# Kernel tuning notes

Hardware: AMD Instinct MI355X
Metric: run time of the kernel (lower is better)

The kernel has to match this reference:

```python
import jax, jax.numpy as jnp
import numpy as np

KEEP_PROB = 0.3
KH, KW = 3, 3
STRIDE = (1, 1)
PADDING = ((1, 1), (1, 1))
DILATION = (1, 1)


def setup_inputs() -> dict:
    key = jax.random.key(0)
    k_x, k_w, k_m, k_b = jax.random.split(key, 4)
    B, C_in, H, W = 16, 64, 112, 112
    C_out = 128
    K = C_in * KH * KW  # 576
    x = jax.random.normal(k_x, (B, C_in, H, W), dtype=jnp.float32)
    weight = jax.random.normal(k_w, (C_out, K), dtype=jnp.float32)
    # binary sparsity pattern of the COO tensor, as a float mask
    mask = (jax.random.uniform(k_m, (C_out, K)) < KEEP_PROB).astype(jnp.float32)
    bias = jax.random.normal(k_b, (C_out,), dtype=jnp.float32)
    return {"x": x, "weight": weight, "mask": mask, "bias": bias}


def reference(x, weight, mask, bias):
    # Effective sparse weight matrix [C_out, C_in*kH*kW]
    spW = weight * mask
    # im2col (F.unfold): patches -> [B, C_in*kH*kW, H_out, W_out]
    # ordering of the K axis is (c, i, j) channel-major, matching torch unfold
    patches = jax.lax.conv_general_dilated_patches(
        x,
        filter_shape=(KH, KW),
        window_strides=STRIDE,
        padding=PADDING,
        rhs_dilation=DILATION,
    )  # [B, K, H_out, W_out]
    # sparse.mm(spW, X) + fold(1x1)  ==  GEMM over the K axis
    out = jnp.einsum('ok,bkhw->bohw', spW, patches)
    out = out + bias[None, :, None, None]
    return out
```

## Files before the change

### kernel.cpp

```cpp
#include <hip/hip_runtime.h>
#include <hip/hip_bf16.h>

#define C_IN    64
#define C_OUT   128
#define HH      112
#define WW      112
#define NB      16
#define KTOT    576
#define NSTEPS  36
#define NPIX    (HH*WW)
#define PH      114
#define PPIX    (PH*PH)
#define XT_OFF  147456
#define XT_BYTES ((size_t)NB * PPIX * C_IN * 2)
#define BAND_H  14
#define BH_X    18
#define B_RECS  288
#define A_BYTES 73728
#define B_BYTES 36864
#define TY      8
#define TX      16
#define HALO_X  18
#define HALO_P  180
#define TILES_X 7
#define NTILES  98

typedef __bf16 bf16x8 __attribute__((ext_vector_type(8)));
typedef float  f32x16 __attribute__((ext_vector_type(16)));

static __device__ __forceinline__ unsigned short f2bf(float v) {
    unsigned int u = __builtin_bit_cast(unsigned int, v);
    u = u + 0x7fffu + ((u >> 16) & 1u);
    return (unsigned short)(u >> 16);
}

#define GLOAD_LDS(gp, lp) __builtin_amdgcn_global_load_lds( \
    (const __attribute__((address_space(1))) void*)(gp),    \
    (__attribute__((address_space(3))) void*)(lp), 16, 0, 0)

__global__ __launch_bounds__(256) void pack_w_kernel(
        const float* __restrict__ weight, const float* __restrict__ mask,
        unsigned short* __restrict__ pw) {
    int t  = blockIdx.x;
    int mt = threadIdx.x >> 6;
    int l  = threadIdx.x & 63;
    int g  = l >> 5;
    int m  = mt * 32 + (l & 31);
    unsigned int words[4];
    #pragma unroll
    for (int ew = 0; ew < 4; ++ew) {
        unsigned int w2[2];
        #pragma unroll
        for (int h = 0; h < 2; ++h) {
            int e    = ew * 2 + h;
            int klog = t * 16 + g * 8 + e;
            int ij   = klog >> 6;
            int c    = klog & 63;
            int ko   = c * 9 + ij;
            w2[h] = f2bf(weight[m * KTOT + ko] * mask[m * KTOT + ko]);
        }
        words[ew] = w2[0] | (w2[1] << 16);
    }
    uint4 o4; o4.x = words[0]; o4.y = words[1]; o4.z = words[2]; o4.w = words[3];
    ((uint4*)pw)[(t * 4 + mt) * 64 + l] = o4;
}

__global__ __launch_bounds__(256) void transpose_x_kernel(
        const float* __restrict__ x, unsigned short* __restrict__ xT) {
    const int b  = blockIdx.y;
    const int pp = blockIdx.x * 256 + threadIdx.x;
    if (pp >= PPIX) return;
    const int hp = pp / PH, wp = pp - hp * PH;
    const int gh = hp - 1, gw = wp - 1;
    const bool valid = (unsigned)gh < (unsigned)HH && (unsigned)gw < (unsigned)WW;
    const float* src = x + (size_t)b * C_IN * (HH * WW) + (gh * WW + gw);
    uint4* dst = (uint4*)(xT + ((size_t)b * PPIX + pp) * C_IN);
    #pragma unroll
    for (int cb = 0; cb < 8; ++cb) {
        unsigned int w4[4];
        #pragma unroll
        for (int h = 0; h < 4; ++h) {
            float v0 = valid ? src[(size_t)(cb * 8 + h * 2    ) * (HH * WW)] : 0.0f;
            float v1 = valid ? src[(size_t)(cb * 8 + h * 2 + 1) * (HH * WW)] : 0.0f;
            w4[h] = (unsigned)f2bf(v0) | ((unsigned)f2bf(v1) << 16);
        }
        uint4 o; o.x = w4[0]; o.y = w4[1]; o.z = w4[2]; o.w = w4[3];
        dst[cb] = o;
    }
}

__global__ __launch_bounds__(448, 1) void sparse_conv_band_kernel(
        const unsigned short* __restrict__ xT, const unsigned short* __restrict__ pw,
        const float* __restrict__ bias, float* __restrict__ out) {
    __shared__ __align__(16) unsigned char smem[A_BYTES + 2 * B_BYTES];
    unsigned char* As  = smem;
    unsigned char* Bs0 = smem + A_BYTES;
    unsigned char* Bs1 = smem + A_BYTES + B_BYTES;

    const int bid  = (blockIdx.x & 7) * 32 + (blockIdx.x >> 3);
    const int b    = bid >> 4;
    const int rem  = bid & 15;
    const int mh   = rem & 1;
    const int band = rem >> 1;
    const int h0   = band * BAND_H;
    const int tid  = threadIdx.x;
    const int wave = tid >> 6, l = tid & 63;
    const int g = l >> 5, ln = l & 31;

    const char* xTb = (const char*)xT + (size_t)b * PPIX * (C_IN * 2);

    {
        const char* pwb = (const char*)pw;
        #pragma unroll
        for (int r = 0; r < 10; ++r) {
            int c  = r * 448 + tid;
            int t  = c >> 7;
            int mt = (c >> 6) & 1;
            int ll = c & 63;
            const char* gp = pwb + (size_t)((t * 4 + mh * 2 + mt) * 64 + ll) * 16;
            GLOAD_LDS(gp, (char*)As + r * 7168 + wave * 1024);
        }
        if (tid < 128) {
            int c  = 10 * 448 + tid;
            int t  = c >> 7;
            int mt = (c >> 6) & 1;
            int ll = c & 63;
            const char* gp = pwb + (size_t)((t * 4 + mh * 2 + mt) * 64 + ll) * 16;
            GLOAD_LDS(gp, (char*)As + 10 * 7168 + wave * 1024);
        }
    }

    auto STAGE = [&](int it, unsigned char* dst) {
        const int w0 = it * 16;
        #pragma unroll
        for (int r = 0; r < 5; ++r) {
            int chunk = r * 448 + tid;
            int p = chunk >> 3, s = chunk & 7;
            int yy = p / BH_X, xx = p - yy * BH_X;
            const char* gp = xTb + (size_t)((h0 + yy) * PH + (w0 + xx)) * (C_IN * 2)
                                 + (((s ^ p) & 7) << 4);
            GLOAD_LDS(gp, (char*)dst + r * 7168 + wave * 1024);
        }
        if (tid < 64) {
            int chunk = 5 * 448 + tid;
            int p = chunk >> 3, s = chunk & 7;
            int yy = p / BH_X, xx = p - yy * BH_X;
            const char* gp = xTb + (size_t)((h0 + yy) * PH + (w0 + xx)) * (C_IN * 2)
                                 + (((s ^ p) & 7) << 4);
            GLOAD_LDS(gp, (char*)dst + 5 * 7168 + wave * 1024);
        }
    };

    const int py = 2 * wave + (ln >> 4);
    const int px = ln & 15;

    float bv[2][16];
    #pragma unroll
    for (int mt = 0; mt < 2; ++mt)
        #pragma unroll
        for (int r = 0; r < 16; ++r) {
            int mloc = (r & 3) + 8 * (r >> 2) + 4 * g;
            bv[mt][r] = bias[mh * 64 + mt * 32 + mloc];
        }

    STAGE(0, Bs0);
    __syncthreads();

    const size_t outb = (size_t)b * C_OUT * NPIX;

    #pragma unroll 1
    for (int it = 0; it < 7; ++it) {
        unsigned char* curB = (it & 1) ? Bs1 : Bs0;
        unsigned char* nxtB = (it & 1) ? Bs0 : Bs1;
        if (it < 6) STAGE(it + 1, nxtB);

        f32x16 acc[2];
        #pragma unroll
        for (int mt = 0; mt < 2; ++mt)
            #pragma unroll
            for (int r = 0; r < 16; ++r) acc[mt][r] = bv[mt][r];

        #pragma unroll
        for (int t = 0; t < NSTEPS; ++t) {
            const int ij = t >> 2, cs = t & 3;
            const int di = ij / 3, dj = ij - di * 3;
            const int jb = cs * 2 + g;
            bf16x8 a0 = __builtin_bit_cast(bf16x8,
                *(const uint4*)(As + ((t * 2 + 0) * 64 + l) * 16));
            bf16x8 a1 = __builtin_bit_cast(bf16x8,
                *(const uint4*)(As + ((t * 2 + 1) * 64 + l) * 16));
            const int Pa = (py + di) * BH_X + (px + dj);
            bf16x8 bb = __builtin_bit_cast(bf16x8,
                *(const uint4*)(curB + Pa * 128 + (((jb ^ Pa) & 7) << 4)));
            acc[0] = __builtin_amdgcn_mfma_f32_32x32x16_bf16(a0, bb, acc[0], 0, 0, 0);
            acc[1] = __builtin_amdgcn_mfma_f32_32x32x16_bf16(a1, bb, acc[1], 0, 0, 0);
        }

        #pragma unroll
        for (int mt = 0; mt < 2; ++mt)
            #pragma unroll
            for (int r = 0; r < 16; ++r) {
                int mloc = (r & 3) + 8 * (r >> 2) + 4 * g;
                int o = mh * 64 + mt * 32 + mloc;
                out[outb + (size_t)o * NPIX + (h0 + py) * WW + it * 16 + px] = acc[mt][r];
            }

        if (it < 6) __syncthreads();
    }
}

__global__ __launch_bounds__(256, 4) void sparse_conv_fb_kernel(
        const float* __restrict__ x, const unsigned short* __restrict__ pw,
        const float* __restrict__ bias, float* __restrict__ out) {
    __shared__ __align__(16) unsigned short xs[HALO_P * C_IN];

    const int bid = blockIdx.x;
    const int b   = bid / NTILES;
    const int t98 = bid % NTILES;
    const int tyi = t98 / TILES_X;
    const int txi = t98 % TILES_X;
    const int h0  = tyi * TY, w0 = txi * TX;
    const int tid = threadIdx.x;

    const float* xb = x + (size_t)b * C_IN * HH * WW;
    {
        const int p  = tid;
        const bool act = p < HALO_P;
        int yy = p / HALO_X;
        int xx = p - yy * HALO_X;
        int gh = h0 + yy - 1, gw = w0 + xx - 1;
        const bool valid = act && (unsigned)gh < (unsigned)HH && (unsigned)gw < (unsigned)WW;
        const float* bp = xb + (gh * WW + gw);
        float v[C_IN];
        #pragma unroll
        for (int c = 0; c < C_IN; ++c)
            v[c] = valid ? bp[c * (HH * WW)] : 0.0f;
        if (act) {
            char* xc = (char*)xs + p * (C_IN * 2);
            #pragma unroll
            for (int j = 0; j < 8; ++j) {
                bf16x8 bvv;
                #pragma unroll
                for (int e = 0; e < 8; ++e) bvv[e] = (__bf16)v[j * 8 + e];
                *(uint4*)(xc + (((j ^ p) & 7) << 4)) = __builtin_bit_cast(uint4, bvv);
            }
        }
    }
    __syncthreads();

    const int wave = tid >> 6, l = tid & 63;
    const int wm = wave >> 1, wn = wave & 1;
    const int g  = l >> 5,  ln = l & 31;

    int P0[2];
    #pragma unroll
    for (int ntp = 0; ntp < 2; ++ntp) {
        int pt = wn * 64 + ntp * 32 + ln;
        P0[ntp] = (pt >> 4) * HALO_X + (pt & 15);
    }

    f32x16 acc[2][2];
    #pragma unroll
    for (int i = 0; i < 2; ++i)
        #pragma unroll
        for (int jq = 0; jq < 2; ++jq)
            #pragma unroll
            for (int q = 0; q < 16; ++q) acc[i][jq][q] = 0.0f;

    const uint4* __restrict__ pwv = (const uint4*)pw;

    #pragma unroll 1
    for (int ij = 0; ij < 9; ++ij) {
        const int di = ij / 3;
        const int dj = ij - di * 3;
        const int P0a = P0[0] + di * HALO_X + dj;
        const int P1a = P0[1] + di * HALO_X + dj;
        #pragma unroll
        for (int cs = 0; cs < 4; ++cs) {
            const int t = ij * 4 + cs;
            bf16x8 a0 = __builtin_bit_cast(bf16x8, pwv[(t * 4 + wm * 2 + 0) * 64 + l]);
            bf16x8 a1 = __builtin_bit_cast(bf16x8, pwv[(t * 4 + wm * 2 + 1) * 64 + l]);
            const int jb = cs * 2 + g;
            bf16x8 b0 = __builtin_bit_cast(bf16x8,
                *(const uint4*)((const char*)xs + P0a * (C_IN * 2) + (((jb ^ P0a) & 7) << 4)));
            bf16x8 b1 = __builtin_bit_cast(bf16x8,
                *(const uint4*)((const char*)xs + P1a * (C_IN * 2) + (((jb ^ P1a) & 7) << 4)));
            acc[0][0] = __builtin_amdgcn_mfma_f32_32x32x16_bf16(a0, b0, acc[0][0], 0, 0, 0);
            acc[0][1] = __builtin_amdgcn_mfma_f32_32x32x16_bf16(a0, b1, acc[0][1], 0, 0, 0);
            acc[1][0] = __builtin_amdgcn_mfma_f32_32x32x16_bf16(a1, b0, acc[1][0], 0, 0, 0);
            acc[1][1] = __builtin_amdgcn_mfma_f32_32x32x16_bf16(a1, b1, acc[1][1], 0, 0, 0);
        }
    }

    const size_t outb = (size_t)b * C_OUT * HH * WW;
    #pragma unroll
    for (int mtp = 0; mtp < 2; ++mtp) {
        #pragma unroll
        for (int r = 0; r < 16; ++r) {
            int mloc = (r & 3) + 8 * (r >> 2) + 4 * g;
            int o = (wm * 2 + mtp) * 32 + mloc;
            float bvv = bias[o];
            #pragma unroll
            for (int ntp = 0; ntp < 2; ++ntp) {
                int p  = wn * 64 + ntp * 32 + ln;
                int gh = h0 + (p >> 4), gw = w0 + (p & 15);
                out[outb + ((size_t)o * HH + gh) * WW + gw] = acc[mtp][ntp][r] + bvv;
            }
        }
    }
}

extern "C" void kernel_launch(void* const* d_in, const int* in_sizes, int n_in,
                              void* d_out, int out_size, void* d_ws, size_t ws_size,
                              hipStream_t stream) {
    const float* x    = (const float*)d_in[0];
    const float* w    = (const float*)d_in[1];
    const float* mk   = (const float*)d_in[2];
    const float* bs   = (const float*)d_in[3];
    float* out        = (float*)d_out;
    unsigned short* pw = (unsigned short*)d_ws;

    pack_w_kernel<<<dim3(NSTEPS), dim3(256), 0, stream>>>(w, mk, pw);

    if (ws_size >= (size_t)XT_OFF + XT_BYTES) {
        unsigned short* xT = (unsigned short*)((char*)d_ws + XT_OFF);
        transpose_x_kernel<<<dim3((PPIX + 255) / 256, NB), dim3(256), 0, stream>>>(x, xT);
        sparse_conv_band_kernel<<<dim3(256), dim3(448), 0, stream>>>(xT, pw, bs, out);
    } else {
        sparse_conv_fb_kernel<<<dim3(NB * NTILES), dim3(256), 0, stream>>>(x, pw, bs, out);
    }
}
```

Baseline: 72.24 us.

## Split output channels into quarters, keep weights in registers, widen transpose parallelism

The main conv kernel now gives each block a quarter of the output channels (32) rather than half. Each lane holds its 36 weight fragments in VGPRs, so the 72KB LDS weight buffer is gone and only the double-buffered input band stays in LDS. The grid doubles to 512 blocks for better CU coverage, but every input band is now staged twice as often and each B fragment feeds one MFMA instead of two. The weight packing is changed to a row-major layout, and the transpose kernel uses 8 threads per padded pixel for more parallelism.

```diff
diff --git a/kernel.cpp b/kernel.cpp
--- a/kernel.cpp
+++ b/kernel.cpp
@@ -16,7 +16,6 @@
 #define BAND_H  14
 #define BH_X    18
 #define B_RECS  288
-#define A_BYTES 73728
 #define B_BYTES 36864
 #define TY      8
 #define TX      16
@@ -41,94 +40,68 @@
 __global__ __launch_bounds__(256) void pack_w_kernel(
         const float* __restrict__ weight, const float* __restrict__ mask,
         unsigned short* __restrict__ pw) {
-    int t  = blockIdx.x;
-    int mt = threadIdx.x >> 6;
-    int l  = threadIdx.x & 63;
-    int g  = l >> 5;
-    int m  = mt * 32 + (l & 31);
-    unsigned int words[4];
-    #pragma unroll
-    for (int ew = 0; ew < 4; ++ew) {
-        unsigned int w2[2];
-        #pragma unroll
-        for (int h = 0; h < 2; ++h) {
-            int e    = ew * 2 + h;
-            int klog = t * 16 + g * 8 + e;
-            int ij   = klog >> 6;
-            int c    = klog & 63;
-            int ko   = c * 9 + ij;
-            w2[h] = f2bf(weight[m * KTOT + ko] * mask[m * KTOT + ko]);
-        }
-        words[ew] = w2[0] | (w2[1] << 16);
-    }
-    uint4 o4; o4.x = words[0]; o4.y = words[1]; o4.z = words[2]; o4.w = words[3];
-    ((uint4*)pw)[(t * 4 + mt) * 64 + l] = o4;
+    const int m   = blockIdx.x;
+    const int tid = threadIdx.x;
+    #pragma unroll
+    for (int base = 0; base < 512; base += 256) {
+        int klog = base + tid;
+        int c = klog & 63, ij = klog >> 6;
+        int ko = c * 9 + ij;
+        pw[m * KTOT + klog] = f2bf(weight[m * KTOT + ko] * mask[m * KTOT + ko]);
+    }
+    if (tid < 64) {
+        int klog = 512 + tid;
+        int c = klog & 63, ij = klog >> 6;
+        int ko = c * 9 + ij;
+        pw[m * KTOT + klog] = f2bf(weight[m * KTOT + ko] * mask[m * KTOT + ko]);
+    }
 }
 
 __global__ __launch_bounds__(256) void transpose_x_kernel(
         const float* __restrict__ x, unsigned short* __restrict__ xT) {
-    const int b  = blockIdx.y;
-    const int pp = blockIdx.x * 256 + threadIdx.x;
-    if (pp >= PPIX) return;
-    const int hp = pp / PH, wp = pp - hp * PH;
+    const int b   = blockIdx.y;
+    const int idx = blockIdx.x * 256 + threadIdx.x;
+    if (idx >= PPIX * 8) return;
+    const int rec = idx >> 3, s = idx & 7;
+    const int hp = rec / PH, wp = rec - hp * PH;
     const int gh = hp - 1, gw = wp - 1;
     const bool valid = (unsigned)gh < (unsigned)HH && (unsigned)gw < (unsigned)WW;
-    const float* src = x + (size_t)b * C_IN * (HH * WW) + (gh * WW + gw);
-    uint4* dst = (uint4*)(xT + ((size_t)b * PPIX + pp) * C_IN);
-    #pragma unroll
-    for (int cb = 0; cb < 8; ++cb) {
-        unsigned int w4[4];
-        #pragma unroll
-        for (int h = 0; h < 4; ++h) {
-            float v0 = valid ? src[(size_t)(cb * 8 + h * 2    ) * (HH * WW)] : 0.0f;
-            float v1 = valid ? src[(size_t)(cb * 8 + h * 2 + 1) * (HH * WW)] : 0.0f;
-            w4[h] = (unsigned)f2bf(v0) | ((unsigned)f2bf(v1) << 16);
-        }
-        uint4 o; o.x = w4[0]; o.y = w4[1]; o.z = w4[2]; o.w = w4[3];
-        dst[cb] = o;
-    }
-}
-
-__global__ __launch_bounds__(448, 1) void sparse_conv_band_kernel(
+    const float* src = x + (size_t)b * C_IN * (HH * WW) + (size_t)(s * 8) * (HH * WW)
+                         + (gh * WW + gw);
+    unsigned int w4[4];
+    #pragma unroll
+    for (int h = 0; h < 4; ++h) {
+        float v0 = valid ? src[(size_t)(h * 2    ) * (HH * WW)] : 0.0f;
+        float v1 = valid ? src[(size_t)(h * 2 + 1) * (HH * WW)] : 0.0f;
+        w4[h] = (unsigned)f2bf(v0) | ((unsigned)f2bf(v1) << 16);
+    }
+    uint4 o; o.x = w4[0]; o.y = w4[1]; o.z = w4[2]; o.w = w4[3];
+    ((uint4*)(xT + ((size_t)b * PPIX + rec) * C_IN))[s] = o;
+}
+
+__global__ __launch_bounds__(448, 1) void sparse_conv_mq_kernel(
         const unsigned short* __restrict__ xT, const unsigned short* __restrict__ pw,
         const float* __restrict__ bias, float* __restrict__ out) {
-    __shared__ __align__(16) unsigned char smem[A_BYTES + 2 * B_BYTES];
-    unsigned char* As  = smem;
-    unsigned char* Bs0 = smem + A_BYTES;
-    unsigned char* Bs1 = smem + A_BYTES + B_BYTES;
-
-    const int bid  = (blockIdx.x & 7) * 32 + (blockIdx.x >> 3);
-    const int b    = bid >> 4;
-    const int rem  = bid & 15;
-    const int mh   = rem & 1;
-    const int band = rem >> 1;
+    __shared__ __align__(16) unsigned char Bs[2][B_BYTES];
+
+    const int bid  = (blockIdx.x & 7) * 64 + (blockIdx.x >> 3);
+    const int b    = bid >> 5;
+    const int rem  = bid & 31;
+    const int mq   = rem & 3;
+    const int band = rem >> 2;
     const int h0   = band * BAND_H;
     const int tid  = threadIdx.x;
     const int wave = tid >> 6, l = tid & 63;
     const int g = l >> 5, ln = l & 31;
 
     const char* xTb = (const char*)xT + (size_t)b * PPIX * (C_IN * 2);
-
-    {
-        const char* pwb = (const char*)pw;
-        #pragma unroll
-        for (int r = 0; r < 10; ++r) {
-            int c  = r * 448 + tid;
-            int t  = c >> 7;
-            int mt = (c >> 6) & 1;
-            int ll = c & 63;
-            const char* gp = pwb + (size_t)((t * 4 + mh * 2 + mt) * 64 + ll) * 16;
-            GLOAD_LDS(gp, (char*)As + r * 7168 + wave * 1024);
-        }
-        if (tid < 128) {
-            int c  = 10 * 448 + tid;
-            int t  = c >> 7;
-            int mt = (c >> 6) & 1;
-            int ll = c & 63;
-            const char* gp = pwb + (size_t)((t * 4 + mh * 2 + mt) * 64 + ll) * 16;
-            GLOAD_LDS(gp, (char*)As + 10 * 7168 + wave * 1024);
-        }
-    }
+    const uint4* __restrict__ pwv = (const uint4*)pw;
+
+    const int m = mq * 32 + ln;
+    uint4 Areg[NSTEPS];
+    #pragma unroll
+    for (int t = 0; t < NSTEPS; ++t)
+        Areg[t] = pwv[(size_t)m * 72 + t * 2 + g];
 
     auto STAGE = [&](int it, unsigned char* dst) {
         const int w0 = it * 16;
@@ -154,56 +127,46 @@
     const int py = 2 * wave + (ln >> 4);
     const int px = ln & 15;
 
-    float bv[2][16];
-    #pragma unroll
-    for (int mt = 0; mt < 2; ++mt)
-        #pragma unroll
-        for (int r = 0; r < 16; ++r) {
-            int mloc = (r & 3) + 8 * (r >> 2) + 4 * g;
-            bv[mt][r] = bias[mh * 64 + mt * 32 + mloc];
-        }
-
-    STAGE(0, Bs0);
+    float bv[16];
+    #pragma unroll
+    for (int r = 0; r < 16; ++r) {
+        int mloc = (r & 3) + 8 * (r >> 2) + 4 * g;
+        bv[r] = bias[mq * 32 + mloc];
+    }
+
+    STAGE(0, Bs[0]);
     __syncthreads();
 
     const size_t outb = (size_t)b * C_OUT * NPIX;
 
     #pragma unroll 1
     for (int it = 0; it < 7; ++it) {
-        unsigned char* curB = (it & 1) ? Bs1 : Bs0;
-        unsigned char* nxtB = (it & 1) ? Bs0 : Bs1;
+        unsigned char* curB = Bs[it & 1];
+        unsigned char* nxtB = Bs[(it & 1) ^ 1];
         if (it < 6) STAGE(it + 1, nxtB);
 
-        f32x16 acc[2];
-        #pragma unroll
-        for (int mt = 0; mt < 2; ++mt)
-            #pragma unroll
-            for (int r = 0; r < 16; ++r) acc[mt][r] = bv[mt][r];
+        f32x16 acc;
+        #pragma unroll
+        for (int r = 0; r < 16; ++r) acc[r] = bv[r];
 
         #pragma unroll
         for (int t = 0; t < NSTEPS; ++t) {
             const int ij = t >> 2, cs = t & 3;
             const int di = ij / 3, dj = ij - di * 3;
             const int jb = cs * 2 + g;
-            bf16x8 a0 = __builtin_bit_cast(bf16x8,
-                *(const uint4*)(As + ((t * 2 + 0) * 64 + l) * 16));
-            bf16x8 a1 = __builtin_bit_cast(bf16x8,
-                *(const uint4*)(As + ((t * 2 + 1) * 64 + l) * 16));
             const int Pa = (py + di) * BH_X + (px + dj);
             bf16x8 bb = __builtin_bit_cast(bf16x8,
                 *(const uint4*)(curB + Pa * 128 + (((jb ^ Pa) & 7) << 4)));
-            acc[0] = __builtin_amdgcn_mfma_f32_32x32x16_bf16(a0, bb, acc[0], 0, 0, 0);
-            acc[1] = __builtin_amdgcn_mfma_f32_32x32x16_bf16(a1, bb, acc[1], 0, 0, 0);
-        }
-
-        #pragma unroll
-        for (int mt = 0; mt < 2; ++mt)
-            #pragma unroll
-            for (int r = 0; r < 16; ++r) {
-                int mloc = (r & 3) + 8 * (r >> 2) + 4 * g;
-                int o = mh * 64 + mt * 32 + mloc;
-                out[outb + (size_t)o * NPIX + (h0 + py) * WW + it * 16 + px] = acc[mt][r];
-            }
+            bf16x8 a = __builtin_bit_cast(bf16x8, Areg[t]);
+            acc = __builtin_amdgcn_mfma_f32_32x32x16_bf16(a, bb, acc, 0, 0, 0);
+        }
+
+        #pragma unroll
+        for (int r = 0; r < 16; ++r) {
+            int mloc = (r & 3) + 8 * (r >> 2) + 4 * g;
+            int o = mq * 32 + mloc;
+            out[outb + (size_t)o * NPIX + (h0 + py) * WW + it * 16 + px] = acc[r];
+        }
 
         if (it < 6) __syncthreads();
     }
@@ -268,6 +231,8 @@
             for (int q = 0; q < 16; ++q) acc[i][jq][q] = 0.0f;
 
     const uint4* __restrict__ pwv = (const uint4*)pw;
+    const int m0 = (wm * 2 + 0) * 32 + ln;
+    const int m1 = (wm * 2 + 1) * 32 + ln;
 
     #pragma unroll 1
     for (int ij = 0; ij < 9; ++ij) {
@@ -278,8 +243,8 @@
         #pragma unroll
         for (int cs = 0; cs < 4; ++cs) {
             const int t = ij * 4 + cs;
-            bf16x8 a0 = __builtin_bit_cast(bf16x8, pwv[(t * 4 + wm * 2 + 0) * 64 + l]);
-            bf16x8 a1 = __builtin_bit_cast(bf16x8, pwv[(t * 4 + wm * 2 + 1) * 64 + l]);
+            bf16x8 a0 = __builtin_bit_cast(bf16x8, pwv[(size_t)m0 * 72 + t * 2 + g]);
+            bf16x8 a1 = __builtin_bit_cast(bf16x8, pwv[(size_t)m1 * 72 + t * 2 + g]);
             const int jb = cs * 2 + g;
             bf16x8 b0 = __builtin_bit_cast(bf16x8,
                 *(const uint4*)((const char*)xs + P0a * (C_IN * 2) + (((jb ^ P0a) & 7) << 4)));
@@ -320,12 +285,12 @@
     float* out        = (float*)d_out;
     unsigned short* pw = (unsigned short*)d_ws;
 
-    pack_w_kernel<<<dim3(NSTEPS), dim3(256), 0, stream>>>(w, mk, pw);
+    pack_w_kernel<<<dim3(C_OUT), dim3(256), 0, stream>>>(w, mk, pw);
 
     if (ws_size >= (size_t)XT_OFF + XT_BYTES) {
         unsigned short* xT = (unsigned short*)((char*)d_ws + XT_OFF);
-        transpose_x_kernel<<<dim3((PPIX + 255) / 256, NB), dim3(256), 0, stream>>>(x, xT);
-        sparse_conv_band_kernel<<<dim3(256), dim3(448), 0, stream>>>(xT, pw, bs, out);
+        transpose_x_kernel<<<dim3((PPIX * 8 + 255) / 256, NB), dim3(256), 0, stream>>>(x, xT);
+        sparse_conv_mq_kernel<<<dim3(512), dim3(448), 0, stream>>>(xT, pw, bs, out);
     } else {
         sparse_conv_fb_kernel<<<dim3(NB * NTILES), dim3(256), 0, stream>>>(x, pw, bs, out);
     }
```

Measured after the change: 76.34 us. 5.7% more time.
